# Optimization experiments

Measured on AMD Instinct MI355X. Metric: run time of the kernel, lower is better.

## Reference

```python
import jax, jax.numpy as jnp
import numpy as np

T, B, H = 512, 64, 1024

def setup_inputs() -> dict:
    key = jax.random.key(0)
    ks = jax.random.split(key, 16)
    names_mat = ['W_ir', 'W_hr', 'W_iz', 'W_hz', 'W_in', 'W_hn']
    names_vec = ['b_ir', 'b_hr', 'b_iz', 'b_hz', 'b_in', 'b_hn']
    inp = {
        'input_': jax.random.normal(ks[0], (T, B, H), dtype=jnp.float32),
        'hidden0': jax.random.normal(ks[1], (B, H), dtype=jnp.float32),
    }
    for i, n in enumerate(names_mat):
        inp[n] = jax.random.normal(ks[2 + i], (H, H), dtype=jnp.float32)
    for i, n in enumerate(names_vec):
        inp[n] = jax.random.normal(ks[8 + i], (H,), dtype=jnp.float32)
    # W = randn(H) * T, b = randn(1) in the original forward; made explicit here
    inp['W_out'] = jax.random.normal(ks[14], (H,), dtype=jnp.float32) * T
    inp['b_out'] = jax.random.normal(ks[15], (1,), dtype=jnp.float32)
    return inp

def reference(input_, hidden0, W_ir, W_hr, W_iz, W_hz, W_in, W_hn,
              b_ir, b_hr, b_iz, b_hz, b_in, b_hn, W_out, b_out):
    h = input_.shape[2]
    # permutation matrix is identity -> lower = tril(ones)
    lower = jnp.tril(jnp.ones((h, h), dtype=input_.dtype))
    Wir, Whr = W_ir * lower, W_hr * lower
    Wiz, Whz = W_iz * lower, W_hz * lower
    Win, Whn = W_in * lower, W_hn * lower

    def step(hid, x):
        # mask == x in the original call: cell(x, lower, x, hidden)
        r = jax.nn.sigmoid(x @ Wir + b_ir * x + hid @ Whr + b_hr)
        z = jax.nn.sigmoid(x @ Wiz + b_iz * x + hid @ Whz + b_hz)
        n = jnp.tanh(x @ Win + b_in * x + r * (hid @ Whn + b_hn))
        hid_new = hid * z + (1.0 - z) * n
        label = jax.nn.sigmoid(hid_new * W_out + b_out) * x  # [B, H]
        return hid_new, label

    _, labels = jax.lax.scan(step, hidden0, input_)  # labels: [T, B, H]
    ans_f = jnp.max(labels, axis=-1)                 # [T, B]
    ans = jnp.where(ans_f >= 0.5, 1, -1).astype(jnp.int32)
    return ans
```

## Files before the change

### kernel.cpp

```cpp
#include <hip/hip_runtime.h>

#define T_DIM 512
#define B_DIM 64
#define H_DIM 1024
#define KSLOT 33
#define APITCH 1032
#define AHEAD 6

typedef __attribute__((ext_vector_type(8))) short bf16x8;
typedef __attribute__((ext_vector_type(4))) float f32x4;


__device__ __forceinline__ unsigned short f2bf(float f) {
    unsigned u = __float_as_uint(f);
    unsigned r = (u + 0x7FFFu + ((u >> 16) & 1u)) >> 16;
    return (unsigned short)r;
}
__device__ __forceinline__ unsigned pack2(float a, float b) {
    return (unsigned)f2bf(a) | ((unsigned)f2bf(b) << 16);
}

__global__ __launch_bounds__(128) void prep_pack(
    const float* __restrict__ Wir, const float* __restrict__ Wiz, const float* __restrict__ Win,
    const float* __restrict__ Whr, const float* __restrict__ Whz, const float* __restrict__ Whn,
    unsigned short* __restrict__ Wpk)
{
    const float* srcs[6] = {Wir, Wiz, Win, Whr, Whz, Whn};
    const int t    = threadIdx.x;
    const int jtks = blockIdx.x;
    const int g    = blockIdx.y;
    const int jt   = jtks >> 5, ks = jtks & 31;
    const int lane = t >> 1, e0 = (t & 1) * 4;
    const float* src = srcs[g];
    const int j  = jt * 16 + (lane & 15);
    const int kb = ks * 32 + (lane >> 4) * 8 + e0;
    ushort4 o; unsigned short* po = (unsigned short*)&o;
    #pragma unroll
    for (int i = 0; i < 4; ++i) {
        const int k = kb + i;
        const float w = (k >= j) ? src[(size_t)k * H_DIM + j] : 0.0f;
        po[i] = f2bf(w);
    }
    const size_t idx = ((((size_t)jt * KSLOT + ks) * 6 + g) * 64 + lane) * 8 + e0;
    *(ushort4*)(Wpk + idx) = o;
}

__global__ __launch_bounds__(256) void init_h(const float* __restrict__ h0,
                                              unsigned short* __restrict__ hring,
                                              unsigned* __restrict__ prog)
{
    if (blockIdx.x < 256) {
        const int i = blockIdx.x * 256 + threadIdx.x;
        hring[i] = f2bf(h0[i]);
    } else {
        #pragma unroll
        for (int k = 0; k < 16; ++k) prog[threadIdx.x + 256 * k] = 0u;
    }
}

__global__ __launch_bounds__(512) void gru_main(
    const float* __restrict__ x,
    const unsigned short* __restrict__ Wpk,
    const float* __restrict__ bir, const float* __restrict__ bhr,
    const float* __restrict__ biz, const float* __restrict__ bhz,
    const float* __restrict__ bin_, const float* __restrict__ bhn,
    const float* __restrict__ Wout, const float* __restrict__ bout,
    const float* __restrict__ h0,
    unsigned short* __restrict__ hring,
    float* __restrict__ pmax,
    unsigned* __restrict__ prog)
{
    __shared__ __align__(16) unsigned short axf[16 * APITCH];
    __shared__ __align__(16) unsigned short ahf[16 * APITCH];
    __shared__ float red[8][6][64][4];
    __shared__ float hown[16][17];
    __shared__ unsigned short hb[16][16];

    const int tid  = threadIdx.x;
    const int lane = tid & 63;
    const int wv   = tid >> 6;

    const int jt = blockIdx.x & 63;
    const int bg = blockIdx.x >> 6;
    const int b0 = bg * 16;

    const int ksb   = jt >> 1;
    const int kcol0 = ksb * 32;
    const int CHN   = (H_DIM - kcol0) >> 3;
    const int cnt   = 32 - ksb;
    const int kpw   = (cnt + 7) >> 3;
    const int ks_s  = ksb + wv * kpw;
    const int ks_e  = (ks_s + kpw < 32) ? (ks_s + kpw) : 32;

    const int row = lane & 15;
    const int kg  = lane >> 4;
    const unsigned short* pax = &axf[row * APITCH + kg * 8];
    const unsigned short* pah = &ahf[row * APITCH + kg * 8];
    const unsigned short* pw0 = Wpk + (size_t)jt * KSLOT * 3072 + lane * 8;

    const int ecol = tid & 15;
    const int eb   = tid >> 4;
    const int ej   = 16 * jt + ecol;
    float c_bir = 0, c_bhr = 0, c_biz = 0, c_bhz = 0, c_bin = 0, c_bhn = 0, c_wo = 0, bo = 0;
    if (tid < 256) {
        c_bir = bir[ej]; c_bhr = bhr[ej]; c_biz = biz[ej]; c_bhz = bhz[ej];
        c_bin = bin_[ej]; c_bhn = bhn[ej]; c_wo = Wout[ej]; bo = bout[0];
    }

    unsigned* myflag = prog + ((bg << 6) + jt) * 16;
    unsigned* pollp  = prog + ((bg << 6) + lane) * 16;

    if (tid < 256) hown[eb][ecol] = h0[(size_t)(b0 + eb) * H_DIM + ej];
    #pragma unroll
    for (int rr = 0; rr < 2; ++rr) {
        const int r = 2 * wv + rr;
        const float* src = x + (size_t)(b0 + r) * H_DIM + kcol0;
        #pragma unroll
        for (int s = 0; s < 2; ++s) {
            const int c8 = lane + (s << 6);
            if (c8 < CHN) {
                const float4 v0 = *(const float4*)(src + c8 * 8);
                const float4 v1 = *(const float4*)(src + c8 * 8 + 4);
                uint4 o = make_uint4(pack2(v0.x, v0.y), pack2(v0.z, v0.w),
                                     pack2(v1.x, v1.y), pack2(v1.z, v1.w));
                *(uint4*)&axf[r * APITCH + c8 * 8] = o;
            }
        }
    }

    unsigned cachedf = 0;

    for (int t = 0; t < T_DIM; ++t) {
        const int slot_r = t & 7, slot_w = (t + 1) & 7;

        if (wv == 0) {
            const int kt = lane;
            int thr;
            if (kt > jt) thr = t;
            else if (kt < jt) thr = t - AHEAD;
            else thr = -0x40000000;
            if (!__all((int)cachedf >= thr)) {
                for (;;) {
                    cachedf = __hip_atomic_load(pollp, __ATOMIC_RELAXED,
                                                __HIP_MEMORY_SCOPE_AGENT);
                    if (__all((int)cachedf >= thr)) break;
                    __builtin_amdgcn_s_sleep(2);
                }
            }
        }
        __syncthreads();

        {
            const unsigned short* base = hring + ((size_t)slot_r * B_DIM + b0) * H_DIM + kcol0;
            const int r0 = 2 * wv, r1 = 2 * wv + 1;
            const int cA = lane, cB = lane + 64;
            const bool gB = (cB < CHN);
            const bool gA = (cA < CHN);
            uint4 o0, o1, o2, o3;
            const unsigned short* a0 = base + (size_t)r0 * H_DIM + cA * 8;
            const unsigned short* a1 = base + (size_t)r0 * H_DIM + cB * 8;
            const unsigned short* a2 = base + (size_t)r1 * H_DIM + cA * 8;
            const unsigned short* a3 = base + (size_t)r1 * H_DIM + cB * 8;
            if (gA) asm volatile("global_load_dwordx4 %0, %1, off sc0 sc1" : "=v"(o0) : "v"(a0));
            if (gB) asm volatile("global_load_dwordx4 %0, %1, off sc0 sc1" : "=v"(o1) : "v"(a1));
            if (gA) asm volatile("global_load_dwordx4 %0, %1, off sc0 sc1" : "=v"(o2) : "v"(a2));
            if (gB) asm volatile("global_load_dwordx4 %0, %1, off sc0 sc1" : "=v"(o3) : "v"(a3));
            asm volatile("s_waitcnt vmcnt(0)" ::: "memory");
            if (gA) *(uint4*)&ahf[r0 * APITCH + cA * 8] = o0;
            if (gB) *(uint4*)&ahf[r0 * APITCH + cB * 8] = o1;
            if (gA) *(uint4*)&ahf[r1 * APITCH + cA * 8] = o2;
            if (gB) *(uint4*)&ahf[r1 * APITCH + cB * 8] = o3;
        }
        __syncthreads();

        f32x4 a0 = 0.f, a1 = 0.f, a2 = 0.f, a3 = 0.f, a4 = 0.f, a5 = 0.f;
        for (int ks = ks_s; ks < ks_e; ++ks) {
            const int off = (ks - ksb) * 32;
            const bf16x8 ax = *(const bf16x8*)(pax + off);
            const bf16x8 ah = *(const bf16x8*)(pah + off);
            const unsigned short* pw = pw0 + (size_t)ks * 3072;
            const bf16x8 w0 = *(const bf16x8*)(pw);
            const bf16x8 w1 = *(const bf16x8*)(pw + 512);
            const bf16x8 w2 = *(const bf16x8*)(pw + 1024);
            const bf16x8 w3 = *(const bf16x8*)(pw + 1536);
            const bf16x8 w4 = *(const bf16x8*)(pw + 2048);
            const bf16x8 w5 = *(const bf16x8*)(pw + 2560);
            a0 = __builtin_amdgcn_mfma_f32_16x16x32_bf16(ax, w0, a0, 0, 0, 0);
            a1 = __builtin_amdgcn_mfma_f32_16x16x32_bf16(ax, w1, a1, 0, 0, 0);
            a2 = __builtin_amdgcn_mfma_f32_16x16x32_bf16(ax, w2, a2, 0, 0, 0);
            a3 = __builtin_amdgcn_mfma_f32_16x16x32_bf16(ah, w3, a3, 0, 0, 0);
            a4 = __builtin_amdgcn_mfma_f32_16x16x32_bf16(ah, w4, a4, 0, 0, 0);
            a5 = __builtin_amdgcn_mfma_f32_16x16x32_bf16(ah, w5, a5, 0, 0, 0);
        }
        *(f32x4*)&red[wv][0][lane][0] = a0;
        *(f32x4*)&red[wv][1][lane][0] = a1;
        *(f32x4*)&red[wv][2][lane][0] = a2;
        *(f32x4*)&red[wv][3][lane][0] = a3;
        *(f32x4*)&red[wv][4][lane][0] = a4;
        *(f32x4*)&red[wv][5][lane][0] = a5;
        __syncthreads();

        if (tid < 256) {
            const int lp = ((eb >> 2) << 4) | ecol;
            const int rg = eb & 3;
            float s0 = 0, s1 = 0, s2 = 0, s3 = 0, s4 = 0, s5 = 0;
            #pragma unroll
            for (int w2i = 0; w2i < 8; ++w2i) {
                s0 += red[w2i][0][lp][rg]; s1 += red[w2i][1][lp][rg];
                s2 += red[w2i][2][lp][rg]; s3 += red[w2i][3][lp][rg];
                s4 += red[w2i][4][lp][rg]; s5 += red[w2i][5][lp][rg];
            }
            const float xv = x[(size_t)t * B_DIM * H_DIM + (size_t)(b0 + eb) * H_DIM + ej];
            const float hv = hown[eb][ecol];
            const float rp = s0 + c_bir * xv + c_bhr + s3;
            const float zp = s1 + c_biz * xv + c_bhz + s4;
            const float r  = 1.0f / (1.0f + expf(-rp));
            const float z  = 1.0f / (1.0f + expf(-zp));
            const float np = s2 + c_bin * xv + r * (s5 + c_bhn);
            const float n  = tanhf(np);
            const float hnew = hv * z + (1.0f - z) * n;
            hown[eb][ecol] = hnew;
            hb[eb][ecol] = f2bf(hnew);
            float lab = (1.0f / (1.0f + expf(-(hnew * c_wo + bo)))) * xv;
            #pragma unroll
            for (int off = 8; off; off >>= 1)
                lab = fmaxf(lab, __shfl_xor(lab, off));
            if (ecol == 0) pmax[((size_t)t * B_DIM + b0 + eb) * 64 + jt] = lab;
        }
        __syncthreads();

        if (wv == 0) {
            #pragma unroll
            for (int pp = 0; pp < 2; ++pp) {
                const int i = lane + (pp << 6);
                const int b = i >> 3, cq = i & 7;
                const unsigned val = (unsigned)hb[b][2 * cq]
                                   | ((unsigned)hb[b][2 * cq + 1] << 16);
                unsigned* dst = (unsigned*)(hring +
                    ((size_t)slot_w * B_DIM + b0 + b) * H_DIM + 16 * jt) + cq;
                __hip_atomic_store(dst, val, __ATOMIC_RELAXED, __HIP_MEMORY_SCOPE_AGENT);
            }
            if (lane == 0)
                __hip_atomic_store(myflag, (unsigned)(t + 1),
                                   __ATOMIC_RELEASE, __HIP_MEMORY_SCOPE_AGENT);
        } else if (t < T_DIM - 1) {
            const float* xs = x + (size_t)(t + 1) * B_DIM * H_DIM;
            for (int r = wv - 1; r < 16; r += 7) {
                const float* src = xs + (size_t)(b0 + r) * H_DIM + kcol0;
                #pragma unroll
                for (int s = 0; s < 2; ++s) {
                    const int c8 = lane + (s << 6);
                    if (c8 < CHN) {
                        const float4 v0 = *(const float4*)(src + c8 * 8);
                        const float4 v1 = *(const float4*)(src + c8 * 8 + 4);
                        uint4 o = make_uint4(pack2(v0.x, v0.y), pack2(v0.z, v0.w),
                                             pack2(v1.x, v1.y), pack2(v1.z, v1.w));
                        *(uint4*)&axf[r * APITCH + c8 * 8] = o;
                    }
                }
            }
        }
    }
}

__global__ __launch_bounds__(256) void finalize(const float* __restrict__ pmax, int* __restrict__ out)
{
    const int i = blockIdx.x * 256 + threadIdx.x;
    if (i >= T_DIM * B_DIM) return;
    const float4* pm = (const float4*)(pmax + (size_t)i * 64);
    float m = -3.4e38f;
    #pragma unroll
    for (int q = 0; q < 16; ++q) {
        const float4 v = pm[q];
        m = fmaxf(m, fmaxf(fmaxf(v.x, v.y), fmaxf(v.z, v.w)));
    }
    out[i] = (m >= 0.5f) ? 1 : -1;
}

extern "C" void kernel_launch(void* const* d_in, const int* in_sizes, int n_in,
                              void* d_out, int out_size, void* d_ws, size_t ws_size,
                              hipStream_t stream)
{
    const float* x    = (const float*)d_in[0];
    const float* h0   = (const float*)d_in[1];
    const float* W_ir = (const float*)d_in[2];
    const float* W_hr = (const float*)d_in[3];
    const float* W_iz = (const float*)d_in[4];
    const float* W_hz = (const float*)d_in[5];
    const float* W_in = (const float*)d_in[6];
    const float* W_hn = (const float*)d_in[7];
    const float* b_ir = (const float*)d_in[8];
    const float* b_hr = (const float*)d_in[9];
    const float* b_iz = (const float*)d_in[10];
    const float* b_hz = (const float*)d_in[11];
    const float* b_in = (const float*)d_in[12];
    const float* b_hn = (const float*)d_in[13];
    const float* W_out = (const float*)d_in[14];
    const float* b_out = (const float*)d_in[15];

    unsigned short* Wpk   = (unsigned short*)d_ws;
    unsigned short* hring = Wpk + (size_t)64 * KSLOT * 3072;
    float* pmax = (float*)(hring + (size_t)8 * B_DIM * H_DIM);
    unsigned* prog = (unsigned*)(pmax + (size_t)T_DIM * B_DIM * 64);

    prep_pack<<<dim3(64 * 32, 6), 128, 0, stream>>>(W_ir, W_iz, W_in, W_hr, W_hz, W_hn, Wpk);
    init_h<<<dim3(257), 256, 0, stream>>>(h0, hring, prog);

    void* args[] = {(void*)&x, (void*)&Wpk,
                    (void*)&b_ir, (void*)&b_hr, (void*)&b_iz, (void*)&b_hz,
                    (void*)&b_in, (void*)&b_hn, (void*)&W_out, (void*)&b_out,
                    (void*)&h0, (void*)&hring, (void*)&pmax, (void*)&prog};
    hipError_t rc = hipLaunchCooperativeKernel((const void*)gru_main, dim3(256), dim3(512),
                                               args, 0, stream);
    (void)rc;

    finalize<<<dim3(T_DIM * B_DIM / 256), 256, 0, stream>>>(pmax, (int*)d_out);
}
```

Measured before the change: 6.404 ms.

## Repartition GRU blocks to 32-column tiles with 8 batch rows and deeper ring

Work is split into 32-column output tiles per block with 8 batch rows per block instead of 16-column tiles with 16 rows. Each block's two 16-column subtiles are handled by separate wave groups, and the MFMA rows 8-15 are padded with zeros. The hidden-state ring grows from 8 to 64 slots and the lookahead allowance rises to 62, so blocks stall less waiting on lagging producers. The h writeback now uses 128 threads followed by a block barrier before the flag store. The trade-off is half-wasted MFMA rows and a larger ring buffer in workspace.

```diff
diff --git a/kernel.cpp b/kernel.cpp
--- a/kernel.cpp
+++ b/kernel.cpp
@@ -3,9 +3,11 @@
 #define T_DIM 512
 #define B_DIM 64
 #define H_DIM 1024
+#define NBLK 32
+#define RING 64
+#define AHEAD 62
 #define KSLOT 33
 #define APITCH 1032
-#define AHEAD 6
 
 typedef __attribute__((ext_vector_type(8))) short bf16x8;
 typedef __attribute__((ext_vector_type(4))) float f32x4;
@@ -26,14 +28,17 @@
     unsigned short* __restrict__ Wpk)
 {
     const float* srcs[6] = {Wir, Wiz, Win, Whr, Whz, Whn};
+    const int bid   = blockIdx.x;
+    const int g     = blockIdx.y;
+    const int jt    = bid >> 6;
+    const int jtile = (bid >> 5) & 1;
+    const int ksrel = bid & 31;
+    if (ksrel >= NBLK - jt) return;
     const int t    = threadIdx.x;
-    const int jtks = blockIdx.x;
-    const int g    = blockIdx.y;
-    const int jt   = jtks >> 5, ks = jtks & 31;
     const int lane = t >> 1, e0 = (t & 1) * 4;
     const float* src = srcs[g];
-    const int j  = jt * 16 + (lane & 15);
-    const int kb = ks * 32 + (lane >> 4) * 8 + e0;
+    const int j  = 32 * jt + 16 * jtile + (lane & 15);
+    const int kb = (jt + ksrel) * 32 + (lane >> 4) * 8 + e0;
     ushort4 o; unsigned short* po = (unsigned short*)&o;
     #pragma unroll
     for (int i = 0; i < 4; ++i) {
@@ -41,7 +46,7 @@
         const float w = (k >= j) ? src[(size_t)k * H_DIM + j] : 0.0f;
         po[i] = f2bf(w);
     }
-    const size_t idx = ((((size_t)jt * KSLOT + ks) * 6 + g) * 64 + lane) * 8 + e0;
+    const size_t idx = ((((size_t)(jt * 2 + jtile) * KSLOT + ksrel) * 6 + g) * 64 + lane) * 8 + e0;
     *(ushort4*)(Wpk + idx) = o;
 }
 
@@ -70,51 +75,53 @@
     float* __restrict__ pmax,
     unsigned* __restrict__ prog)
 {
-    __shared__ __align__(16) unsigned short axf[16 * APITCH];
-    __shared__ __align__(16) unsigned short ahf[16 * APITCH];
+    __shared__ __align__(16) unsigned short axf[8 * APITCH];
+    __shared__ __align__(16) unsigned short ahf[8 * APITCH];
+    __shared__ __align__(16) unsigned short zblk[8];
     __shared__ float red[8][6][64][4];
-    __shared__ float hown[16][17];
-    __shared__ unsigned short hb[16][16];
+    __shared__ float hown[8][33];
+    __shared__ unsigned short hb[8][32];
 
     const int tid  = threadIdx.x;
     const int lane = tid & 63;
     const int wv   = tid >> 6;
 
-    const int jt = blockIdx.x & 63;
-    const int bg = blockIdx.x >> 6;
-    const int b0 = bg * 16;
-
-    const int ksb   = jt >> 1;
-    const int kcol0 = ksb * 32;
+    const int jt = blockIdx.x & 31;
+    const int bg = blockIdx.x >> 5;
+    const int b0 = bg * 8;
+
+    const int kcol0 = 32 * jt;
     const int CHN   = (H_DIM - kcol0) >> 3;
-    const int cnt   = 32 - ksb;
-    const int kpw   = (cnt + 7) >> 3;
-    const int ks_s  = ksb + wv * kpw;
-    const int ks_e  = (ks_s + kpw < 32) ? (ks_s + kpw) : 32;
+    const int cnt   = NBLK - jt;
+    const int jtile = wv >> 2;
+    const int ws4   = wv & 3;
+    const int kpw   = (cnt + 3) >> 2;
+    const int ks_s  = jt + ws4 * kpw;
+    const int ks_e  = (ks_s + kpw < NBLK) ? (ks_s + kpw) : NBLK;
 
     const int row = lane & 15;
     const int kg  = lane >> 4;
-    const unsigned short* pax = &axf[row * APITCH + kg * 8];
-    const unsigned short* pah = &ahf[row * APITCH + kg * 8];
-    const unsigned short* pw0 = Wpk + (size_t)jt * KSLOT * 3072 + lane * 8;
-
-    const int ecol = tid & 15;
-    const int eb   = tid >> 4;
-    const int ej   = 16 * jt + ecol;
+    const unsigned short* pax = (row < 8) ? &axf[row * APITCH + kg * 8] : zblk;
+    const unsigned short* pah = (row < 8) ? &ahf[row * APITCH + kg * 8] : zblk;
+    const int astride = (row < 8) ? 32 : 0;
+    const unsigned short* pw0 = Wpk + (size_t)(jt * 2 + jtile) * KSLOT * 3072 + lane * 8;
+
+    const int ecol = tid & 31;
+    const int eb   = tid >> 5;
+    const int ej   = 32 * jt + ecol;
     float c_bir = 0, c_bhr = 0, c_biz = 0, c_bhz = 0, c_bin = 0, c_bhn = 0, c_wo = 0, bo = 0;
     if (tid < 256) {
         c_bir = bir[ej]; c_bhr = bhr[ej]; c_biz = biz[ej]; c_bhz = bhz[ej];
         c_bin = bin_[ej]; c_bhn = bhn[ej]; c_wo = Wout[ej]; bo = bout[0];
     }
 
-    unsigned* myflag = prog + ((bg << 6) + jt) * 16;
-    unsigned* pollp  = prog + ((bg << 6) + lane) * 16;
-
+    unsigned* myflag = prog + ((bg << 5) + jt) * 16;
+    unsigned* pollp  = prog + ((bg << 5) + (lane & 31)) * 16;
+
+    if (tid < 8) zblk[tid] = 0;
     if (tid < 256) hown[eb][ecol] = h0[(size_t)(b0 + eb) * H_DIM + ej];
-    #pragma unroll
-    for (int rr = 0; rr < 2; ++rr) {
-        const int r = 2 * wv + rr;
-        const float* src = x + (size_t)(b0 + r) * H_DIM + kcol0;
+    {
+        const float* src = x + (size_t)(b0 + wv) * H_DIM + kcol0;
         #pragma unroll
         for (int s = 0; s < 2; ++s) {
             const int c8 = lane + (s << 6);
@@ -123,7 +130,7 @@
                 const float4 v1 = *(const float4*)(src + c8 * 8 + 4);
                 uint4 o = make_uint4(pack2(v0.x, v0.y), pack2(v0.z, v0.w),
                                      pack2(v1.x, v1.y), pack2(v1.z, v1.w));
-                *(uint4*)&axf[r * APITCH + c8 * 8] = o;
+                *(uint4*)&axf[wv * APITCH + c8 * 8] = o;
             }
         }
     }
@@ -131,10 +138,10 @@
     unsigned cachedf = 0;
 
     for (int t = 0; t < T_DIM; ++t) {
-        const int slot_r = t & 7, slot_w = (t + 1) & 7;
+        const int slot_r = t & (RING - 1), slot_w = (t + 1) & (RING - 1);
 
         if (wv == 0) {
-            const int kt = lane;
+            const int kt = lane & 31;
             int thr;
             if (kt > jt) thr = t;
             else if (kt < jt) thr = t - AHEAD;
@@ -151,34 +158,27 @@
         __syncthreads();
 
         {
-            const unsigned short* base = hring + ((size_t)slot_r * B_DIM + b0) * H_DIM + kcol0;
-            const int r0 = 2 * wv, r1 = 2 * wv + 1;
+            const unsigned short* base = hring +
+                ((size_t)slot_r * B_DIM + b0 + wv) * H_DIM + kcol0;
             const int cA = lane, cB = lane + 64;
-            const bool gB = (cB < CHN);
-            const bool gA = (cA < CHN);
-            uint4 o0, o1, o2, o3;
-            const unsigned short* a0 = base + (size_t)r0 * H_DIM + cA * 8;
-            const unsigned short* a1 = base + (size_t)r0 * H_DIM + cB * 8;
-            const unsigned short* a2 = base + (size_t)r1 * H_DIM + cA * 8;
-            const unsigned short* a3 = base + (size_t)r1 * H_DIM + cB * 8;
+            const bool gA = (cA < CHN), gB = (cB < CHN);
+            uint4 o0, o1;
+            const unsigned short* a0 = base + cA * 8;
+            const unsigned short* a1 = base + cB * 8;
             if (gA) asm volatile("global_load_dwordx4 %0, %1, off sc0 sc1" : "=v"(o0) : "v"(a0));
             if (gB) asm volatile("global_load_dwordx4 %0, %1, off sc0 sc1" : "=v"(o1) : "v"(a1));
-            if (gA) asm volatile("global_load_dwordx4 %0, %1, off sc0 sc1" : "=v"(o2) : "v"(a2));
-            if (gB) asm volatile("global_load_dwordx4 %0, %1, off sc0 sc1" : "=v"(o3) : "v"(a3));
             asm volatile("s_waitcnt vmcnt(0)" ::: "memory");
-            if (gA) *(uint4*)&ahf[r0 * APITCH + cA * 8] = o0;
-            if (gB) *(uint4*)&ahf[r0 * APITCH + cB * 8] = o1;
-            if (gA) *(uint4*)&ahf[r1 * APITCH + cA * 8] = o2;
-            if (gB) *(uint4*)&ahf[r1 * APITCH + cB * 8] = o3;
+            if (gA) *(uint4*)&ahf[wv * APITCH + cA * 8] = o0;
+            if (gB) *(uint4*)&ahf[wv * APITCH + cB * 8] = o1;
         }
         __syncthreads();
 
         f32x4 a0 = 0.f, a1 = 0.f, a2 = 0.f, a3 = 0.f, a4 = 0.f, a5 = 0.f;
         for (int ks = ks_s; ks < ks_e; ++ks) {
-            const int off = (ks - ksb) * 32;
+            const int off = (ks - jt) * astride;
             const bf16x8 ax = *(const bf16x8*)(pax + off);
             const bf16x8 ah = *(const bf16x8*)(pah + off);
-            const unsigned short* pw = pw0 + (size_t)ks * 3072;
+            const unsigned short* pw = pw0 + (size_t)(ks - jt) * 3072;
             const bf16x8 w0 = *(const bf16x8*)(pw);
             const bf16x8 w1 = *(const bf16x8*)(pw + 512);
             const bf16x8 w2 = *(const bf16x8*)(pw + 1024);
@@ -201,14 +201,15 @@
         __syncthreads();
 
         if (tid < 256) {
-            const int lp = ((eb >> 2) << 4) | ecol;
+            const int wb = (ecol >> 4) * 4;
+            const int lp = ((eb >> 2) << 4) | (ecol & 15);
             const int rg = eb & 3;
             float s0 = 0, s1 = 0, s2 = 0, s3 = 0, s4 = 0, s5 = 0;
             #pragma unroll
-            for (int w2i = 0; w2i < 8; ++w2i) {
-                s0 += red[w2i][0][lp][rg]; s1 += red[w2i][1][lp][rg];
-                s2 += red[w2i][2][lp][rg]; s3 += red[w2i][3][lp][rg];
-                s4 += red[w2i][4][lp][rg]; s5 += red[w2i][5][lp][rg];
+            for (int w2i = 0; w2i < 4; ++w2i) {
+                s0 += red[wb + w2i][0][lp][rg]; s1 += red[wb + w2i][1][lp][rg];
+                s2 += red[wb + w2i][2][lp][rg]; s3 += red[wb + w2i][3][lp][rg];
+                s4 += red[wb + w2i][4][lp][rg]; s5 += red[wb + w2i][5][lp][rg];
             }
             const float xv = x[(size_t)t * B_DIM * H_DIM + (size_t)(b0 + eb) * H_DIM + ej];
             const float hv = hown[eb][ecol];
@@ -223,40 +224,36 @@
             hb[eb][ecol] = f2bf(hnew);
             float lab = (1.0f / (1.0f + expf(-(hnew * c_wo + bo)))) * xv;
             #pragma unroll
-            for (int off = 8; off; off >>= 1)
+            for (int off = 16; off; off >>= 1)
                 lab = fmaxf(lab, __shfl_xor(lab, off));
-            if (ecol == 0) pmax[((size_t)t * B_DIM + b0 + eb) * 64 + jt] = lab;
-        }
-        __syncthreads();
-
-        if (wv == 0) {
+            if (ecol == 0) pmax[((size_t)t * B_DIM + b0 + eb) * 32 + jt] = lab;
+        }
+        __syncthreads();
+
+        if (tid < 128) {
+            const int b = tid >> 4, cq = tid & 15;
+            const unsigned val = (unsigned)hb[b][2 * cq] | ((unsigned)hb[b][2 * cq + 1] << 16);
+            unsigned* dst = (unsigned*)(hring +
+                ((size_t)slot_w * B_DIM + b0 + b) * H_DIM + 32 * jt) + cq;
+            __hip_atomic_store(dst, val, __ATOMIC_RELAXED, __HIP_MEMORY_SCOPE_AGENT);
+        }
+        __syncthreads();
+        if (tid == 0)
+            __hip_atomic_store(myflag, (unsigned)(t + 1),
+                               __ATOMIC_RELEASE, __HIP_MEMORY_SCOPE_AGENT);
+
+        if (t < T_DIM - 1) {
+            const float* src = x + (size_t)(t + 1) * B_DIM * H_DIM
+                             + (size_t)(b0 + wv) * H_DIM + kcol0;
             #pragma unroll
-            for (int pp = 0; pp < 2; ++pp) {
-                const int i = lane + (pp << 6);
-                const int b = i >> 3, cq = i & 7;
-                const unsigned val = (unsigned)hb[b][2 * cq]
-                                   | ((unsigned)hb[b][2 * cq + 1] << 16);
-                unsigned* dst = (unsigned*)(hring +
-                    ((size_t)slot_w * B_DIM + b0 + b) * H_DIM + 16 * jt) + cq;
-                __hip_atomic_store(dst, val, __ATOMIC_RELAXED, __HIP_MEMORY_SCOPE_AGENT);
-            }
-            if (lane == 0)
-                __hip_atomic_store(myflag, (unsigned)(t + 1),
-                                   __ATOMIC_RELEASE, __HIP_MEMORY_SCOPE_AGENT);
-        } else if (t < T_DIM - 1) {
-            const float* xs = x + (size_t)(t + 1) * B_DIM * H_DIM;
-            for (int r = wv - 1; r < 16; r += 7) {
-                const float* src = xs + (size_t)(b0 + r) * H_DIM + kcol0;
-                #pragma unroll
-                for (int s = 0; s < 2; ++s) {
-                    const int c8 = lane + (s << 6);
-                    if (c8 < CHN) {
-                        const float4 v0 = *(const float4*)(src + c8 * 8);
-                        const float4 v1 = *(const float4*)(src + c8 * 8 + 4);
-                        uint4 o = make_uint4(pack2(v0.x, v0.y), pack2(v0.z, v0.w),
-                                             pack2(v1.x, v1.y), pack2(v1.z, v1.w));
-                        *(uint4*)&axf[r * APITCH + c8 * 8] = o;
-                    }
+            for (int s = 0; s < 2; ++s) {
+                const int c8 = lane + (s << 6);
+                if (c8 < CHN) {
+                    const float4 v0 = *(const float4*)(src + c8 * 8);
+                    const float4 v1 = *(const float4*)(src + c8 * 8 + 4);
+                    uint4 o = make_uint4(pack2(v0.x, v0.y), pack2(v0.z, v0.w),
+                                         pack2(v1.x, v1.y), pack2(v1.z, v1.w));
+                    *(uint4*)&axf[wv * APITCH + c8 * 8] = o;
                 }
             }
         }
@@ -267,10 +264,10 @@
 {
     const int i = blockIdx.x * 256 + threadIdx.x;
     if (i >= T_DIM * B_DIM) return;
-    const float4* pm = (const float4*)(pmax + (size_t)i * 64);
+    const float4* pm = (const float4*)(pmax + (size_t)i * 32);
     float m = -3.4e38f;
     #pragma unroll
-    for (int q = 0; q < 16; ++q) {
+    for (int q = 0; q < 8; ++q) {
         const float4 v = pm[q];
         m = fmaxf(m, fmaxf(fmaxf(v.x, v.y), fmaxf(v.z, v.w)));
     }
@@ -299,11 +296,11 @@
     const float* b_out = (const float*)d_in[15];
 
     unsigned short* Wpk   = (unsigned short*)d_ws;
-    unsigned short* hring = Wpk + (size_t)64 * KSLOT * 3072;
-    float* pmax = (float*)(hring + (size_t)8 * B_DIM * H_DIM);
-    unsigned* prog = (unsigned*)(pmax + (size_t)T_DIM * B_DIM * 64);
-
-    prep_pack<<<dim3(64 * 32, 6), 128, 0, stream>>>(W_ir, W_iz, W_in, W_hr, W_hz, W_hn, Wpk);
+    unsigned short* hring = Wpk + (size_t)NBLK * 2 * KSLOT * 3072;
+    float* pmax = (float*)(hring + (size_t)RING * B_DIM * H_DIM);
+    unsigned* prog = (unsigned*)(pmax + (size_t)T_DIM * B_DIM * 32);
+
+    prep_pack<<<dim3(NBLK * 64, 6), 128, 0, stream>>>(W_ir, W_iz, W_in, W_hr, W_hz, W_hn, Wpk);
     init_h<<<dim3(257), 256, 0, stream>>>(h0, hring, prog);
 
     void* args[] = {(void*)&x, (void*)&Wpk,
```

Result: faster. 5.701 ms (-11.0%).
